# Performance work log

Measured on AMD Instinct MI355X. Metric: run time of the kernel, lower is better.

## Reference

```python
import jax, jax.numpy as jnp
import numpy as np

B, A, N_IN, N_POINTS = 64, 256, 512, 2048


def _sq_cdist(u, v):
    # |u_i - v_j|^2 via expansion, abs() as in the torch original
    d = -2.0 * (u @ v.T) + (u * u).sum(1)[:, None] + (v * v).sum(1)[None, :]
    return jnp.abs(d)


def setup_inputs() -> dict:
    key = jax.random.key(0)
    k1, k2, k3, k4 = jax.random.split(key, 4)
    x = jax.random.normal(k1, (B, A, N_IN), dtype=jnp.float32)
    atom_mask = jax.random.bernoulli(k2, 0.8, (B, A))  # ragged valid-atom mask
    inducing_points = jax.random.normal(k3, (N_POINTS, N_IN), dtype=jnp.float32)
    gamma = (1.0 + 0.25 * jax.random.normal(k4, (N_IN,), dtype=jnp.float32)) * np.sqrt(N_IN).astype(np.float32)
    return {"x": x, "atom_mask": atom_mask, "inducing_points": inducing_points, "gamma": gamma}


def reference(x, atom_mask, inducing_points, gamma):
    b, a, n_in = x.shape
    m = atom_mask.astype(x.dtype)                      # [B, A]
    mf = m[..., None]                                  # [B, A, 1]
    n = m.sum()
    # masked mean / unbiased std over valid atoms (torch .std is ddof=1)
    mean = (x * mf).sum((0, 1)) / n                    # [n_in]
    var = (((x - mean) ** 2) * mf).sum((0, 1)) / (n - 1.0)
    std = jnp.sqrt(var) + 1e-5                         # [n_in]
    xn = (x - mean) / std * mf                         # zero out padded atoms

    g2 = gamma ** 2 + 0.001                            # [n_in]
    z = (xn / g2).reshape(b * a, n_in)                 # [N, n_in]
    zi = inducing_points / g2                          # [M, n_in]

    Kx = jnp.exp(-_sq_cdist(z, zi))                    # [N, M]
    Kind = jnp.exp(-_sq_cdist(zi, zi))                 # [M, M]
    Kinv = jnp.linalg.inv(Kind + 0.05 * jnp.eye(Kind.shape[0], dtype=x.dtype))

    t = Kx @ Kinv                                      # [N, M]
    x_new = ((t @ inducing_points) * std + mean).reshape(b, a, n_in) * mf
    var_out = (1.0 - (t * Kx).sum(-1)).reshape(b, a) * m
    return x_new, var_out
```

## Files before the change

### kernel.cpp

```cpp
#include <hip/hip_runtime.h>
#include <math.h>
#include <stdint.h>

namespace {

constexpr int NROW = 16384;
constexpr int NF   = 512;
constexpr int MIND = 2048;
constexpr float CC = 0.98f;

typedef _Float16 half8 __attribute__((ext_vector_type(8)));
typedef _Float16 half4v __attribute__((ext_vector_type(4)));
typedef float floatx4 __attribute__((ext_vector_type(4)));

__device__ __forceinline__ void gload16(const void* g, void* l) {
  __builtin_amdgcn_global_load_lds(
      (__attribute__((address_space(1))) void*)g,
      (__attribute__((address_space(3))) void*)l, 16, 0, 0);
}

#define MEMFENCE asm volatile("" ::: "memory")
#define GATE(N) asm volatile("s_waitcnt vmcnt(" #N ")" ::: "memory")

__global__ __launch_bounds__(256) void stats_kernel(
    const float* __restrict__ x, const int* __restrict__ mask,
    float* __restrict__ sum, float* __restrict__ sumsq, float* __restrict__ cnt)
{
  const int t = threadIdx.x;
  const int row0 = blockIdx.x * 64;
  float s0 = 0.f, s1 = 0.f, q0 = 0.f, q1 = 0.f, c = 0.f;
  for (int r = 0; r < 64; ++r) {
    const int row = row0 + r;
    const float m = (mask[row] != 0) ? 1.f : 0.f;
    const float v0 = x[(size_t)row * NF + t];
    const float v1 = x[(size_t)row * NF + t + 256];
    s0 += m * v0; q0 += m * v0 * v0;
    s1 += m * v1; q1 += m * v1 * v1;
    c += m;
  }
  atomicAdd(&sum[t], s0);        atomicAdd(&sum[t + 256], s1);
  atomicAdd(&sumsq[t], q0);      atomicAdd(&sumsq[t + 256], q1);
  if (t == 0) atomicAdd(cnt, c);
}

__global__ __launch_bounds__(256) void finalize_stats(
    const float* __restrict__ sum, const float* __restrict__ sumsq,
    const float* __restrict__ cnt, const float* __restrict__ gamma,
    float* __restrict__ meanv, float* __restrict__ stdv,
    float* __restrict__ zsv, float* __restrict__ giv)
{
  const int f = blockIdx.x * 256 + threadIdx.x;
  const float n = cnt[0];
  const float mu = sum[f] / n;
  const float var = (sumsq[f] - sum[f] * mu) / (n - 1.0f);
  const float sd = sqrtf(var) + 1e-5f;
  const float g = gamma[f];
  const float g2 = g * g + 0.001f;
  meanv[f] = mu;
  stdv[f]  = sd;
  zsv[f]   = 1.0f / (sd * g2);
  giv[f]   = 1.0f / g2;
}

__global__ __launch_bounds__(256) void make_z(
    const float* __restrict__ x, const int* __restrict__ mask,
    const float* __restrict__ ip, const float* __restrict__ meanv,
    const float* __restrict__ zsv, const float* __restrict__ giv,
    _Float16* __restrict__ Zh, _Float16* __restrict__ Zih,
    float* __restrict__ rnorm, float* __restrict__ cnorm)
{
  const int row = blockIdx.x;
  const int t = threadIdx.x;
  float v0, v1;
  if (row < NROW) {
    const float m = (mask[row] != 0) ? 1.f : 0.f;
    v0 = (x[(size_t)row * NF + t      ] - meanv[t      ]) * zsv[t      ] * m;
    v1 = (x[(size_t)row * NF + t + 256] - meanv[t + 256]) * zsv[t + 256] * m;
    const _Float16 h0 = (_Float16)v0, h1 = (_Float16)v1;
    Zh[(size_t)row * NF + t] = h0;
    Zh[(size_t)row * NF + t + 256] = h1;
    v0 = (float)h0; v1 = (float)h1;
  } else {
    const int r = row - NROW;
    v0 = ip[(size_t)r * NF + t      ] * giv[t      ];
    v1 = ip[(size_t)r * NF + t + 256] * giv[t + 256];
    const _Float16 h0 = (_Float16)v0, h1 = (_Float16)v1;
    Zih[(size_t)r * NF + t] = h0;
    Zih[(size_t)r * NF + t + 256] = h1;
    v0 = (float)h0; v1 = (float)h1;
  }
  float nrm = v0 * v0 + v1 * v1;
  #pragma unroll
  for (int off = 32; off; off >>= 1) nrm += __shfl_xor(nrm, off);
  __shared__ float red[4];
  if ((t & 63) == 0) red[t >> 6] = nrm;
  __syncthreads();
  if (t == 0) {
    const float s = red[0] + red[1] + red[2] + red[3];
    if (row < NROW) rnorm[row] = s; else cnorm[row - NROW] = s;
  }
}

template <int PASS>
__global__ __launch_bounds__(512, 2) void mfma_gemm256f(
    const _Float16* __restrict__ A, const _Float16* __restrict__ B, int K,
    const float* __restrict__ rn, const float* __restrict__ cn,
    _Float16* __restrict__ DKout, float* __restrict__ Cf,
    const _Float16* __restrict__ DK, const float* __restrict__ u,
    float* __restrict__ varacc,
    const float* __restrict__ colsumR, const float* __restrict__ stdv,
    const float* __restrict__ meanv, const int* __restrict__ mask)
{
  __shared__ __align__(16) _Float16 Asmem[4][256 * 32];
  __shared__ __align__(16) _Float16 Bsmem[4][256 * 32];

  const int tid = threadIdx.x;
  const int w = tid >> 6, L = tid & 63;
  const int wm = w >> 2, wn = w & 3;
  const int lq = L >> 4, lr = L & 15;
  int bn, bm;
  if constexpr (PASS == 0) {
    const int wgid = blockIdx.y * 8 + blockIdx.x;
    const int xcd = wgid & 7, q = wgid >> 3;
    bm = xcd + 8 * (q >> 3);
    bn = q & 7;
  } else {
    const int wgid = blockIdx.y * 10 + blockIdx.x;
    const int xcd = wgid & 7, q = wgid >> 3;
    bm = xcd + 8 * (q / 10);
    bn = q % 10;
  }
  const int NT = K >> 5;

  const int srow  = tid >> 2;
  const int sslot = tid & 3;
  const int gslot = sslot ^ ((tid >> 3) & 3);
  const _Float16* Ag = A + (size_t)(bm * 256 + srow) * K + gslot * 8;
  const _Float16* Bg = B + (size_t)(bn * 256 + srow) * K + gslot * 8;
  const size_t rstride = (size_t)128 * K;
  const int ldst = srow * 32 + sslot * 8;

  const int fswz = (lq ^ ((lr >> 1) & 3)) * 8;
  const int aoff = (wm * 128 + lr) * 32 + fswz;
  const int boff = (wn * 64  + lr) * 32 + fswz;

  floatx4 acc[8][4] = {};

  auto stageA = [&](int t) {
    _Float16* dst = Asmem[t & 3] + ldst;
    const _Float16* src = Ag + (size_t)t * 32;
    gload16(src, dst);
    gload16(src + rstride, dst + 128 * 32);
  };
  auto stageB = [&](int t) {
    _Float16* dst = Bsmem[t & 3] + ldst;
    const _Float16* src = Bg + (size_t)t * 32;
    gload16(src, dst);
    gload16(src + rstride, dst + 128 * 32);
  };

  stageA(0); stageB(0);
  if (NT > 1) { stageA(1); stageB(1); }
  if (NT > 2) { stageA(2); stageB(2); }
  if (NT > 2)      { GATE(8); }
  else if (NT > 1) { GATE(4); }
  else             { GATE(0); }
  __builtin_amdgcn_s_barrier();
  MEMFENCE;

  for (int t = 0; t < NT; ++t) {
    const _Float16* As = Asmem[t & 3];
    const _Float16* Bs = Bsmem[t & 3];
    half8 af[4], bf[4], af2[4];

    #pragma unroll
    for (int mi = 0; mi < 4; ++mi) af[mi] = *(const half8*)&As[aoff + mi * 512];
    #pragma unroll
    for (int ni = 0; ni < 4; ++ni) bf[ni] = *(const half8*)&Bs[boff + ni * 512];
    if (t + 3 < NT) stageA(t + 3);
    MEMFENCE;
    __builtin_amdgcn_s_barrier();
    MEMFENCE;
    __builtin_amdgcn_s_setprio(1);
    #pragma unroll
    for (int mi = 0; mi < 4; ++mi)
      #pragma unroll
      for (int ni = 0; ni < 4; ++ni)
        acc[mi][ni] = __builtin_amdgcn_mfma_f32_16x16x32_f16(
            af[mi], bf[ni], acc[mi][ni], 0, 0, 0);
    __builtin_amdgcn_s_setprio(0);

    #pragma unroll
    for (int mi = 0; mi < 4; ++mi)
      af2[mi] = *(const half8*)&As[aoff + (mi + 4) * 512];
    if (t + 3 < NT) stageB(t + 3);
    if (t + 4 <= NT)      { GATE(8); }
    else if (t + 3 == NT) { GATE(4); }
    else if (t + 2 == NT) { GATE(0); }
    __builtin_amdgcn_s_barrier();
    MEMFENCE;
    __builtin_amdgcn_s_setprio(1);
    #pragma unroll
    for (int mi = 0; mi < 4; ++mi)
      #pragma unroll
      for (int ni = 0; ni < 4; ++ni)
        acc[mi + 4][ni] = __builtin_amdgcn_mfma_f32_16x16x32_f16(
            af2[mi], bf[ni], acc[mi + 4][ni], 0, 0, 0);
    __builtin_amdgcn_s_setprio(0);
  }

  const int grb = bm * 256 + wm * 128;
  const int gcb = bn * 256 + wn * 64;

  if constexpr (PASS == 0) {
    if (bm < NROW / 256) {
      #pragma unroll
      for (int mi = 0; mi < 8; ++mi)
        #pragma unroll
        for (int e = 0; e < 4; ++e) {
          const int gr = grb + mi * 16 + lq * 4 + e;
          const float rni = rn[gr];
          #pragma unroll
          for (int ni = 0; ni < 4; ++ni) {
            const int gc = gcb + ni * 16 + lr;
            const float d = rni + cn[gc] - 2.f * acc[mi][ni][e];
            DKout[(size_t)gr * MIND + gc] = (_Float16)(expf(-fabsf(d)) - CC);
          }
        }
    } else {
      #pragma unroll
      for (int mi = 0; mi < 8; ++mi)
        #pragma unroll
        for (int e = 0; e < 4; ++e) {
          const int gr = grb + mi * 16 + lq * 4 + e;
          const int gr2 = gr - NROW;
          const float rni = rn[gr];
          #pragma unroll
          for (int ni = 0; ni < 4; ++ni) {
            const int gc = gcb + ni * 16 + lr;
            const float d = rni + cn[gc] - 2.f * acc[mi][ni][e];
            float kx = expf(-fabsf(d));
            if (gr2 == gc) kx += 0.05f;
            Cf[(size_t)gr2 * MIND + gc] = kx;
          }
        }
    }
  } else {
    if (bn < MIND / 256) {
      #pragma unroll
      for (int mi = 0; mi < 8; ++mi)
        #pragma unroll
        for (int e = 0; e < 4; ++e) {
          const int gr = grb + mi * 16 + lq * 4 + e;
          float partial = 0.f;
          #pragma unroll
          for (int ni = 0; ni < 4; ++ni) {
            const int gc = gcb + ni * 16 + lr;
            const float tv = acc[mi][ni][e] + CC * u[gc];
            partial += tv * (CC + (float)DK[(size_t)gr * MIND + gc]);
          }
          partial += __shfl_xor(partial, 1);
          partial += __shfl_xor(partial, 2);
          partial += __shfl_xor(partial, 4);
          partial += __shfl_xor(partial, 8);
          if (lr == 0) atomicAdd(&varacc[gr], partial);
        }
    } else {
      const int gcb3 = (bn - MIND / 256) * 256 + wn * 64;
      #pragma unroll
      for (int mi = 0; mi < 8; ++mi)
        #pragma unroll
        for (int e = 0; e < 4; ++e) {
          const int gr = grb + mi * 16 + lq * 4 + e;
          const float mrow = (mask[gr] != 0) ? 1.f : 0.f;
          #pragma unroll
          for (int ni = 0; ni < 4; ++ni) {
            const int gc3 = gcb3 + ni * 16 + lr;
            const float v = acc[mi][ni][e] + CC * colsumR[gc3];
            Cf[(size_t)gr * NF + gc3] = (v * stdv[gc3] + meanv[gc3]) * mrow;
          }
        }
    }
  }
}

__global__ __launch_bounds__(256) void gemm_f32(
    const float* __restrict__ A, const float* __restrict__ B,
    float* __restrict__ C, int M, int N, int K)
{
  constexpr int BM = 64, BN = 64, BK = 16;
  const int tid = threadIdx.x;
  const int tx = tid % 16, ty = tid / 16;
  const int bn = blockIdx.x, bm = blockIdx.y;
  __shared__ float As[BK][BM + 4];
  __shared__ float Bs[BK][BN + 4];
  float acc[4][4] = {};
  const float* Ag = A + (size_t)bm * BM * K;
  const float* Bg = B + bn * BN;
  for (int k0 = 0; k0 < K; k0 += BK) {
    {
      const int r = tid >> 2, c4 = (tid & 3) << 2;
      const float4 av = *(const float4*)(Ag + (size_t)r * K + k0 + c4);
      As[c4 + 0][r] = av.x; As[c4 + 1][r] = av.y;
      As[c4 + 2][r] = av.z; As[c4 + 3][r] = av.w;
      const int kr = tid / 16, nc = (tid % 16) << 2;
      *(float4*)&Bs[kr][nc] = *(const float4*)(Bg + (size_t)(k0 + kr) * N + nc);
    }
    __syncthreads();
    #pragma unroll
    for (int kk = 0; kk < BK; ++kk) {
      const float4 a4 = *(const float4*)&As[kk][ty * 4];
      const float4 b4 = *(const float4*)&Bs[kk][tx * 4];
      const float a[4] = {a4.x, a4.y, a4.z, a4.w};
      const float b[4] = {b4.x, b4.y, b4.z, b4.w};
      #pragma unroll
      for (int i = 0; i < 4; ++i)
        #pragma unroll
        for (int j = 0; j < 4; ++j) acc[i][j] += a[i] * b[j];
    }
    __syncthreads();
  }
  #pragma unroll
  for (int i = 0; i < 4; ++i) {
    float4 o4; o4.x = acc[i][0]; o4.y = acc[i][1]; o4.z = acc[i][2]; o4.w = acc[i][3];
    *(float4*)(C + (size_t)(bm * BM + ty * 4 + i) * N + bn * BN + tx * 4) = o4;
  }
}


__global__ __launch_bounds__(256) void gj_diag(
    float* __restrict__ A, float* __restrict__ Pall, int k)
{
  const int o = k * 64;
  __shared__ float D[64][68];
  const int t = threadIdx.x;
  #pragma unroll
  for (int l = 0; l < 4; ++l) {
    const int v = t + l * 256;
    const int r = v >> 4, c4 = (v & 15) << 2;
    *(float4*)&D[r][c4] = *(const float4*)(A + (size_t)(o + r) * MIND + o + c4);
  }
  __syncthreads();
  const int i = t >> 2, c0 = (t & 3) * 16;
  for (int s = 0; s < 64; ++s) {
    const float p = 1.0f / D[s][s];
    if (t < 64 && t != s) D[s][t] *= p;
    __syncthreads();
    if (i != s) {
      const float f = D[i][s];
      #pragma unroll
      for (int c = c0; c < c0 + 16; c += 4) {
        float4 ds = *(const float4*)&D[s][c];
        float4 di = *(const float4*)&D[i][c];
        di.x -= f * ds.x; di.y -= f * ds.y; di.z -= f * ds.z; di.w -= f * ds.w;
        *(float4*)&D[i][c] = di;
      }
      if (s >= c0 && s < c0 + 16) D[i][s] = -f * p;
    }
    if (t == 0) D[s][s] = p;
    __syncthreads();
  }
  float* P = Pall + k * 4096;
  #pragma unroll
  for (int l = 0; l < 4; ++l) {
    const int v = t + l * 256;
    const int r = v >> 4, c4 = (v & 15) << 2;
    const float4 dv = *(const float4*)&D[r][c4];
    *(float4*)(P + r * 64 + c4) = dv;
    *(float4*)(A + (size_t)(o + r) * MIND + o + c4) = dv;
  }
}

__global__ __launch_bounds__(256) void gj_prep(
    const float* __restrict__ A, const float* __restrict__ Pall,
    float* __restrict__ CP, float* __restrict__ Bsave, int k)
{
  const int o = k * 64;
  const int t = threadIdx.x;
  if (blockIdx.x >= 32) {
    const int j0 = (blockIdx.x - 32) * 64;
    #pragma unroll
    for (int l = 0; l < 4; ++l) {
      const int v = t + l * 256;
      const int r = v >> 4, c4 = (v & 15) << 2;
      *(float4*)(Bsave + r * MIND + j0 + c4) =
          *(const float4*)(A + (size_t)(o + r) * MIND + j0 + c4);
    }
    return;
  }
  const int i0 = blockIdx.x * 64;
  if (i0 == o) return;
  const float* P = Pall + k * 4096;
  __shared__ float At[64][68];
  __shared__ float Pl[64][68];
  #pragma unroll
  for (int l = 0; l < 4; ++l) {
    const int v = t + l * 256;
    const int r = v >> 4, c4 = (v & 15) << 2;
    const float4 av = *(const float4*)(A + (size_t)(i0 + r) * MIND + o + c4);
    At[c4 + 0][r] = av.x; At[c4 + 1][r] = av.y;
    At[c4 + 2][r] = av.z; At[c4 + 3][r] = av.w;
    *(float4*)&Pl[r][c4] = *(const float4*)(P + r * 64 + c4);
  }
  __syncthreads();
  const int ty = t >> 4, tx = t & 15;
  float acc[4][4] = {};
  for (int s = 0; s < 64; ++s) {
    const float4 a4 = *(const float4*)&At[s][ty * 4];
    const float4 b4 = *(const float4*)&Pl[s][tx * 4];
    const float a[4] = {a4.x, a4.y, a4.z, a4.w};
    const float b[4] = {b4.x, b4.y, b4.z, b4.w};
    #pragma unroll
    for (int i = 0; i < 4; ++i)
      #pragma unroll
      for (int j = 0; j < 4; ++j) acc[i][j] += a[i] * b[j];
  }
  #pragma unroll
  for (int i = 0; i < 4; ++i) {
    float4 o4; o4.x = acc[i][0]; o4.y = acc[i][1]; o4.z = acc[i][2]; o4.w = acc[i][3];
    *(float4*)(CP + (i0 + ty * 4 + i) * 64 + tx * 4) = o4;
  }
}

__global__ __launch_bounds__(256) void gj_apply(
    float* __restrict__ A, float* __restrict__ Pall,
    const float* __restrict__ CP, const float* __restrict__ Bsave, int k)
{
  const int o = k * 64;
  const int i0 = blockIdx.y * 64, j0 = blockIdx.x * 64;
  const int t = threadIdx.x;

  if (i0 == o && j0 == o) return;

  if (j0 == o) {
    #pragma unroll
    for (int l = 0; l < 4; ++l) {
      const int v = t + l * 256;
      const int r = v >> 4, c4 = (v & 15) << 2;
      float4 x = *(const float4*)(CP + (i0 + r) * 64 + c4);
      x.x = -x.x; x.y = -x.y; x.z = -x.z; x.w = -x.w;
      *(float4*)(A + (size_t)(i0 + r) * MIND + o + c4) = x;
    }
    return;
  }

  __shared__ float S1[64 * 68];
  __shared__ float S2[64 * 68];
  #define DD(r, c) S1[(r) * 68 + (c)]

  const bool isrow = (i0 == o);
  const float* Lsrc = isrow ? (Pall + k * 4096) : (CP + i0 * 64);
  #pragma unroll
  for (int l = 0; l < 4; ++l) {
    const int v = t + l * 256;
    const int r = v >> 4, c4 = (v & 15) << 2;
    const float4 lv = *(const float4*)(Lsrc + r * 64 + c4);
    S1[(c4 + 0) * 68 + r] = lv.x; S1[(c4 + 1) * 68 + r] = lv.y;
    S1[(c4 + 2) * 68 + r] = lv.z; S1[(c4 + 3) * 68 + r] = lv.w;
    *(float4*)&S2[r * 68 + c4] = *(const float4*)(Bsave + r * MIND + j0 + c4);
  }
  __syncthreads();
  const int ty = t >> 4, tx = t & 15;
  float acc[4][4] = {};
  for (int s = 0; s < 64; ++s) {
    const float4 a4 = *(const float4*)&S1[s * 68 + ty * 4];
    const float4 b4 = *(const float4*)&S2[s * 68 + tx * 4];
    const float a[4] = {a4.x, a4.y, a4.z, a4.w};
    const float b[4] = {b4.x, b4.y, b4.z, b4.w};
    #pragma unroll
    for (int i = 0; i < 4; ++i)
      #pragma unroll
      for (int j = 0; j < 4; ++j) acc[i][j] += a[i] * b[j];
  }

  if (isrow) {
    #pragma unroll
    for (int i = 0; i < 4; ++i) {
      float4 o4; o4.x = acc[i][0]; o4.y = acc[i][1]; o4.z = acc[i][2]; o4.w = acc[i][3];
      *(float4*)(A + (size_t)(o + ty * 4 + i) * MIND + j0 + tx * 4) = o4;
    }
    return;
  }

  const bool isdiagnext = (i0 == o + 64) && (j0 == o + 64);
  if (!isdiagnext) {
    #pragma unroll
    for (int i = 0; i < 4; ++i) {
      float* cp = A + (size_t)(i0 + ty * 4 + i) * MIND + j0 + tx * 4;
      float4 cv = *(const float4*)cp;
      cv.x -= acc[i][0]; cv.y -= acc[i][1]; cv.z -= acc[i][2]; cv.w -= acc[i][3];
      *(float4*)cp = cv;
    }
    return;
  }

  __syncthreads();
  #pragma unroll
  for (int i = 0; i < 4; ++i) {
    const float4 cv = *(const float4*)(A + (size_t)(i0 + ty * 4 + i) * MIND + j0 + tx * 4);
    DD(ty * 4 + i, tx * 4 + 0) = cv.x - acc[i][0];
    DD(ty * 4 + i, tx * 4 + 1) = cv.y - acc[i][1];
    DD(ty * 4 + i, tx * 4 + 2) = cv.z - acc[i][2];
    DD(ty * 4 + i, tx * 4 + 3) = cv.w - acc[i][3];
  }
  __syncthreads();
  const int di = t >> 2, c0 = (t & 3) * 16;
  for (int s = 0; s < 64; ++s) {
    const float p = 1.0f / DD(s, s);
    if (t < 64 && t != s) DD(s, t) *= p;
    __syncthreads();
    if (di != s) {
      const float f = DD(di, s);
      #pragma unroll
      for (int c = c0; c < c0 + 16; c += 4) {
        float4 ds = *(const float4*)&DD(s, c);
        float4 dv = *(const float4*)&DD(di, c);
        dv.x -= f * ds.x; dv.y -= f * ds.y; dv.z -= f * ds.z; dv.w -= f * ds.w;
        *(float4*)&DD(di, c) = dv;
      }
      if (s >= c0 && s < c0 + 16) DD(di, s) = -f * p;
    }
    if (t == 0) DD(s, s) = p;
    __syncthreads();
  }
  float* Pn = Pall + (k + 1) * 4096;
  #pragma unroll
  for (int l = 0; l < 4; ++l) {
    const int v = t + l * 256;
    const int r = v >> 4, c4 = (v & 15) << 2;
    const float4 dv = *(const float4*)&DD(r, c4);
    *(float4*)(Pn + r * 64 + c4) = dv;
    *(float4*)(A + (size_t)(i0 + r) * MIND + j0 + c4) = dv;
  }
  #undef DD
}

__global__ __launch_bounds__(256) void rowsum_cast(
    const float* __restrict__ Ai, float* __restrict__ u,
    _Float16* __restrict__ Kih)
{
  const int row = blockIdx.x * 4 + (threadIdx.x >> 6);
  const int lane = threadIdx.x & 63;
  const float* src = Ai + (size_t)row * MIND;
  _Float16* dst = Kih + (size_t)row * MIND;
  float s = 0.f;
  #pragma unroll
  for (int it = 0; it < 8; ++it) {
    const int c = it * 256 + lane * 4;
    const float4 v = *(const float4*)(src + c);
    s += v.x + v.y + v.z + v.w;
    half4v h; h.x = (_Float16)v.x; h.y = (_Float16)v.y;
    h.z = (_Float16)v.z; h.w = (_Float16)v.w;
    *(half4v*)(dst + c) = h;
  }
  #pragma unroll
  for (int off = 32; off; off >>= 1) s += __shfl_xor(s, off);
  if (lane == 0) u[row] = s;
}

__global__ __launch_bounds__(256) void transpose_colsum(
    const float* __restrict__ R, _Float16* __restrict__ Rt,
    float* __restrict__ cs)
{
  __shared__ float T[64][65];
  __shared__ float psum[4][64];
  const int j0 = blockIdx.x * 64;
  const int f0 = blockIdx.y * 64;
  const int t = threadIdx.x;
  #pragma unroll
  for (int l = 0; l < 16; ++l) {
    const int idx = t + l * 256;
    T[idx >> 6][idx & 63] = R[(size_t)(j0 + (idx >> 6)) * NF + f0 + (idx & 63)];
  }
  __syncthreads();
  #pragma unroll
  for (int l = 0; l < 16; ++l) {
    const int idx = t + l * 256;
    const int fr = idx >> 6, jc = idx & 63;
    Rt[(size_t)(f0 + fr) * MIND + j0 + jc] = (_Float16)T[jc][fr];
  }
  const int f = t & 63, q = t >> 6;
  float s = 0.f;
  #pragma unroll
  for (int j = q * 16; j < q * 16 + 16; ++j) s += T[j][f];
  psum[q][f] = s;
  __syncthreads();
  if (t < 64) atomicAdd(&cs[f0 + t], psum[0][t] + psum[1][t] + psum[2][t] + psum[3][t]);
}

__global__ __launch_bounds__(256) void var_finalize(
    const float* __restrict__ varacc, const int* __restrict__ mask,
    float* __restrict__ outv)
{
  const int i = blockIdx.x * 256 + threadIdx.x;
  const float m = (mask[i] != 0) ? 1.f : 0.f;
  outv[i] = (1.0f - varacc[i]) * m;
}

}

extern "C" void kernel_launch(void* const* d_in, const int* in_sizes, int n_in,
                              void* d_out, int out_size, void* d_ws, size_t ws_size,
                              hipStream_t stream)
{
  (void)in_sizes; (void)n_in; (void)out_size; (void)ws_size;
  const float* x     = (const float*)d_in[0];
  const int*   mask  = (const int*)d_in[1];
  const float* ip    = (const float*)d_in[2];
  const float* gamma = (const float*)d_in[3];
  float* out = (float*)d_out;

  float* w       = (float*)d_ws;
  float* sum     = w;
  float* sumsq   = w + 512;
  float* cnt     = w + 1024;
  float* varacc  = w + 1536;
  float* colsumR = w + 17920;
  float* meanv   = w + 18432;
  float* stdv    = w + 18944;
  float* zsv     = w + 19456;
  float* giv     = w + 19968;
  float* rnorm   = w + 20480;
  float* cnorm   = w + 36864;
  float* u       = w + 38912;
  float* Ai      = w + 40960;
  float* R       = w + 4235264;
  float* Pall    = w + 5283840;
  float* CP      = w + 5414912;
  float* Bsave   = w + 5545984;
  _Float16* hb   = (_Float16*)(w + 5677056);
  _Float16* Zh   = hb;
  _Float16* Zih  = hb + 8388608;
  _Float16* DK   = hb + 9437184;
  _Float16* Kih  = hb + 42991616;
  _Float16* Rt   = hb + 47185920;

  hipMemsetAsync(w, 0, 18432 * sizeof(float), stream);

  stats_kernel<<<256, 256, 0, stream>>>(x, mask, sum, sumsq, cnt);
  finalize_stats<<<2, 256, 0, stream>>>(sum, sumsq, cnt, gamma, meanv, stdv, zsv, giv);
  make_z<<<NROW + MIND, 256, 0, stream>>>(x, mask, ip, meanv, zsv, giv, Zh, Zih, rnorm, cnorm);

  mfma_gemm256f<0><<<dim3(MIND / 256, (NROW + MIND) / 256), 512, 0, stream>>>(
      Zh, Zih, NF, rnorm, cnorm,
      DK, Ai, nullptr, nullptr, nullptr, nullptr, nullptr, nullptr, nullptr);

  gj_diag<<<1, 256, 0, stream>>>(Ai, Pall, 0);
  gj_prep<<<64, 256, 0, stream>>>(Ai, Pall, CP, Bsave, 0);
  for (int k = 0; k < 32; ++k) {
    gj_apply<<<dim3(32, 32), 256, 0, stream>>>(Ai, Pall, CP, Bsave, k);
    if (k < 31) gj_prep<<<64, 256, 0, stream>>>(Ai, Pall, CP, Bsave, k + 1);
  }

  gemm_f32<<<dim3(NF / 64, MIND / 64), 256, 0, stream>>>(Ai, ip, R, MIND, NF, MIND);
  transpose_colsum<<<dim3(MIND / 64, NF / 64), 256, 0, stream>>>(R, Rt, colsumR);
  rowsum_cast<<<MIND / 4, 256, 0, stream>>>(Ai, u, Kih);

  mfma_gemm256f<1><<<dim3((MIND + NF) / 256, NROW / 256), 512, 0, stream>>>(
      DK, Kih, MIND, nullptr, nullptr,
      nullptr, out, DK, u, varacc, colsumR, stdv, meanv, mask);

  var_finalize<<<NROW / 256, 256, 0, stream>>>(varacc, mask, out + (size_t)NROW * NF);
}
```

Measured before the change: 2.084 ms.

## Fuse Gauss-Jordan inversion steps into one persistent kernel with grid barriers

Replaces the ~66 separate launches of the block Gauss-Jordan inversion, plus the following f32 GEMM, transpose/colsum and rowsum-cast kernels, with one persistent 512-block kernel. Each step is separated by a software grid barrier built on atomics. The goal is to remove per-launch overhead and launch gaps on the serialized inversion chain. In exchange, each block handles two apply tiles per step, and correctness depends on all 512 blocks being co-resident, otherwise the barrier can deadlock. The barrier counters sit in the zeroed workspace area.

Result: slower. 6.857 ms (+229.0%).

```diff
diff --git a/kernel.cpp b/kernel.cpp
--- a/kernel.cpp
+++ b/kernel.cpp
@@ -8,6 +8,7 @@
 constexpr int NF   = 512;
 constexpr int MIND = 2048;
 constexpr float CC = 0.98f;
+constexpr int GJ_BLOCKS = 512;
 
 typedef _Float16 half8 __attribute__((ext_vector_type(8)));
 typedef _Float16 half4v __attribute__((ext_vector_type(4)));
@@ -21,6 +22,27 @@
 
 #define MEMFENCE asm volatile("" ::: "memory")
 #define GATE(N) asm volatile("s_waitcnt vmcnt(" #N ")" ::: "memory")
+
+__device__ __forceinline__ void gbar(int* cnt, int* gen, int nb) {
+  __syncthreads();
+  if (threadIdx.x == 0) {
+    __threadfence();
+    const int g = __hip_atomic_load(gen, __ATOMIC_RELAXED,
+                                    __HIP_MEMORY_SCOPE_AGENT);
+    if (__hip_atomic_fetch_add(cnt, 1, __ATOMIC_ACQ_REL,
+                               __HIP_MEMORY_SCOPE_AGENT) == nb - 1) {
+      __hip_atomic_store(cnt, 0, __ATOMIC_RELAXED, __HIP_MEMORY_SCOPE_AGENT);
+      __hip_atomic_fetch_add(gen, 1, __ATOMIC_RELEASE,
+                             __HIP_MEMORY_SCOPE_AGENT);
+    } else {
+      while (__hip_atomic_load(gen, __ATOMIC_ACQUIRE,
+                               __HIP_MEMORY_SCOPE_AGENT) == g)
+        __builtin_amdgcn_s_sleep(16);
+    }
+    __threadfence();
+  }
+  __syncthreads();
+}
 
 __global__ __launch_bounds__(256) void stats_kernel(
     const float* __restrict__ x, const int* __restrict__ mask,
@@ -284,80 +306,37 @@
   }
 }
 
-__global__ __launch_bounds__(256) void gemm_f32(
-    const float* __restrict__ A, const float* __restrict__ B,
-    float* __restrict__ C, int M, int N, int K)
-{
-  constexpr int BM = 64, BN = 64, BK = 16;
-  const int tid = threadIdx.x;
-  const int tx = tid % 16, ty = tid / 16;
-  const int bn = blockIdx.x, bm = blockIdx.y;
-  __shared__ float As[BK][BM + 4];
-  __shared__ float Bs[BK][BN + 4];
-  float acc[4][4] = {};
-  const float* Ag = A + (size_t)bm * BM * K;
-  const float* Bg = B + bn * BN;
-  for (int k0 = 0; k0 < K; k0 += BK) {
-    {
-      const int r = tid >> 2, c4 = (tid & 3) << 2;
-      const float4 av = *(const float4*)(Ag + (size_t)r * K + k0 + c4);
-      As[c4 + 0][r] = av.x; As[c4 + 1][r] = av.y;
-      As[c4 + 2][r] = av.z; As[c4 + 3][r] = av.w;
-      const int kr = tid / 16, nc = (tid % 16) << 2;
-      *(float4*)&Bs[kr][nc] = *(const float4*)(Bg + (size_t)(k0 + kr) * N + nc);
-    }
-    __syncthreads();
-    #pragma unroll
-    for (int kk = 0; kk < BK; ++kk) {
-      const float4 a4 = *(const float4*)&As[kk][ty * 4];
-      const float4 b4 = *(const float4*)&Bs[kk][tx * 4];
-      const float a[4] = {a4.x, a4.y, a4.z, a4.w};
-      const float b[4] = {b4.x, b4.y, b4.z, b4.w};
-      #pragma unroll
-      for (int i = 0; i < 4; ++i)
-        #pragma unroll
-        for (int j = 0; j < 4; ++j) acc[i][j] += a[i] * b[j];
-    }
-    __syncthreads();
-  }
-  #pragma unroll
-  for (int i = 0; i < 4; ++i) {
-    float4 o4; o4.x = acc[i][0]; o4.y = acc[i][1]; o4.z = acc[i][2]; o4.w = acc[i][3];
-    *(float4*)(C + (size_t)(bm * BM + ty * 4 + i) * N + bn * BN + tx * 4) = o4;
-  }
-}
-
-
-__global__ __launch_bounds__(256) void gj_diag(
-    float* __restrict__ A, float* __restrict__ Pall, int k)
+
+__device__ __forceinline__ void d_gj_diag(
+    float* __restrict__ A, float* __restrict__ Pall, int k, float* S1)
 {
   const int o = k * 64;
-  __shared__ float D[64][68];
   const int t = threadIdx.x;
+  #define D(r, c) S1[(r) * 68 + (c)]
   #pragma unroll
   for (int l = 0; l < 4; ++l) {
     const int v = t + l * 256;
     const int r = v >> 4, c4 = (v & 15) << 2;
-    *(float4*)&D[r][c4] = *(const float4*)(A + (size_t)(o + r) * MIND + o + c4);
+    *(float4*)&D(r, c4) = *(const float4*)(A + (size_t)(o + r) * MIND + o + c4);
   }
   __syncthreads();
   const int i = t >> 2, c0 = (t & 3) * 16;
   for (int s = 0; s < 64; ++s) {
-    const float p = 1.0f / D[s][s];
-    if (t < 64 && t != s) D[s][t] *= p;
+    const float p = 1.0f / D(s, s);
+    if (t < 64 && t != s) D(s, t) *= p;
     __syncthreads();
     if (i != s) {
-      const float f = D[i][s];
+      const float f = D(i, s);
       #pragma unroll
       for (int c = c0; c < c0 + 16; c += 4) {
-        float4 ds = *(const float4*)&D[s][c];
-        float4 di = *(const float4*)&D[i][c];
+        float4 ds = *(const float4*)&D(s, c);
+        float4 di = *(const float4*)&D(i, c);
         di.x -= f * ds.x; di.y -= f * ds.y; di.z -= f * ds.z; di.w -= f * ds.w;
-        *(float4*)&D[i][c] = di;
+        *(float4*)&D(i, c) = di;
       }
-      if (s >= c0 && s < c0 + 16) D[i][s] = -f * p;
-    }
-    if (t == 0) D[s][s] = p;
+      if (s >= c0 && s < c0 + 16) D(i, s) = -f * p;
+    }
+    if (t == 0) D(s, s) = p;
     __syncthreads();
   }
   float* P = Pall + k * 4096;
@@ -365,20 +344,22 @@
   for (int l = 0; l < 4; ++l) {
     const int v = t + l * 256;
     const int r = v >> 4, c4 = (v & 15) << 2;
-    const float4 dv = *(const float4*)&D[r][c4];
+    const float4 dv = *(const float4*)&D(r, c4);
     *(float4*)(P + r * 64 + c4) = dv;
     *(float4*)(A + (size_t)(o + r) * MIND + o + c4) = dv;
   }
-}
-
-__global__ __launch_bounds__(256) void gj_prep(
-    const float* __restrict__ A, const float* __restrict__ Pall,
-    float* __restrict__ CP, float* __restrict__ Bsave, int k)
+  #undef D
+}
+
+__device__ __forceinline__ void d_gj_prep(
+    float* __restrict__ A, float* __restrict__ Pall,
+    float* __restrict__ CP, float* __restrict__ Bsave, int k, int b,
+    float* S1, float* S2)
 {
   const int o = k * 64;
   const int t = threadIdx.x;
-  if (blockIdx.x >= 32) {
-    const int j0 = (blockIdx.x - 32) * 64;
+  if (b >= 32) {
+    const int j0 = (b - 32) * 64;
     #pragma unroll
     for (int l = 0; l < 4; ++l) {
       const int v = t + l * 256;
@@ -388,32 +369,30 @@
     }
     return;
   }
-  const int i0 = blockIdx.x * 64;
+  const int i0 = b * 64;
   if (i0 == o) return;
   const float* P = Pall + k * 4096;
-  __shared__ float At[64][68];
-  __shared__ float Pl[64][68];
   #pragma unroll
   for (int l = 0; l < 4; ++l) {
     const int v = t + l * 256;
     const int r = v >> 4, c4 = (v & 15) << 2;
     const float4 av = *(const float4*)(A + (size_t)(i0 + r) * MIND + o + c4);
-    At[c4 + 0][r] = av.x; At[c4 + 1][r] = av.y;
-    At[c4 + 2][r] = av.z; At[c4 + 3][r] = av.w;
-    *(float4*)&Pl[r][c4] = *(const float4*)(P + r * 64 + c4);
+    S1[(c4 + 0) * 68 + r] = av.x; S1[(c4 + 1) * 68 + r] = av.y;
+    S1[(c4 + 2) * 68 + r] = av.z; S1[(c4 + 3) * 68 + r] = av.w;
+    *(float4*)&S2[r * 68 + c4] = *(const float4*)(P + r * 64 + c4);
   }
   __syncthreads();
   const int ty = t >> 4, tx = t & 15;
   float acc[4][4] = {};
   for (int s = 0; s < 64; ++s) {
-    const float4 a4 = *(const float4*)&At[s][ty * 4];
-    const float4 b4 = *(const float4*)&Pl[s][tx * 4];
+    const float4 a4 = *(const float4*)&S1[s * 68 + ty * 4];
+    const float4 b4 = *(const float4*)&S2[s * 68 + tx * 4];
     const float a[4] = {a4.x, a4.y, a4.z, a4.w};
-    const float b[4] = {b4.x, b4.y, b4.z, b4.w};
+    const float bb[4] = {b4.x, b4.y, b4.z, b4.w};
     #pragma unroll
     for (int i = 0; i < 4; ++i)
       #pragma unroll
-      for (int j = 0; j < 4; ++j) acc[i][j] += a[i] * b[j];
+      for (int j = 0; j < 4; ++j) acc[i][j] += a[i] * bb[j];
   }
   #pragma unroll
   for (int i = 0; i < 4; ++i) {
@@ -422,12 +401,12 @@
   }
 }
 
-__global__ __launch_bounds__(256) void gj_apply(
+__device__ __forceinline__ void d_gj_apply(
     float* __restrict__ A, float* __restrict__ Pall,
-    const float* __restrict__ CP, const float* __restrict__ Bsave, int k)
+    const float* __restrict__ CP, const float* __restrict__ Bsave, int k,
+    int i0, int j0, float* S1, float* S2)
 {
   const int o = k * 64;
-  const int i0 = blockIdx.y * 64, j0 = blockIdx.x * 64;
   const int t = threadIdx.x;
 
   if (i0 == o && j0 == o) return;
@@ -444,10 +423,8 @@
     return;
   }
 
-  __shared__ float S1[64 * 68];
-  __shared__ float S2[64 * 68];
+  __syncthreads();
   #define DD(r, c) S1[(r) * 68 + (c)]
-
   const bool isrow = (i0 == o);
   const float* Lsrc = isrow ? (Pall + k * 4096) : (CP + i0 * 64);
   #pragma unroll
@@ -466,11 +443,11 @@
     const float4 a4 = *(const float4*)&S1[s * 68 + ty * 4];
     const float4 b4 = *(const float4*)&S2[s * 68 + tx * 4];
     const float a[4] = {a4.x, a4.y, a4.z, a4.w};
-    const float b[4] = {b4.x, b4.y, b4.z, b4.w};
+    const float bb[4] = {b4.x, b4.y, b4.z, b4.w};
     #pragma unroll
     for (int i = 0; i < 4; ++i)
       #pragma unroll
-      for (int j = 0; j < 4; ++j) acc[i][j] += a[i] * b[j];
+      for (int j = 0; j < 4; ++j) acc[i][j] += a[i] * bb[j];
   }
 
   if (isrow) {
@@ -523,7 +500,7 @@
     if (t == 0) DD(s, s) = p;
     __syncthreads();
   }
-  float* Pn = Pall + (k + 1) * 4096;
+  float* Pn = Pall + (size_t)(k + 1) * 4096;
   #pragma unroll
   for (int l = 0; l < 4; ++l) {
     const int v = t + l * 256;
@@ -535,11 +512,51 @@
   #undef DD
 }
 
-__global__ __launch_bounds__(256) void rowsum_cast(
+__device__ __forceinline__ void d_gemm_f32(
+    const float* __restrict__ A, const float* __restrict__ B,
+    float* __restrict__ C, int bm, int bn, float* S1, float* S2)
+{
+  constexpr int BK = 16;
+  const int tid = threadIdx.x;
+  const int tx = tid % 16, ty = tid / 16;
+  float acc[4][4] = {};
+  const float* Ag = A + (size_t)bm * 64 * MIND;
+  const float* Bg = B + bn * 64;
+  for (int k0 = 0; k0 < MIND; k0 += BK) {
+    {
+      const int r = tid >> 2, c4 = (tid & 3) << 2;
+      const float4 av = *(const float4*)(Ag + (size_t)r * MIND + k0 + c4);
+      S1[(c4 + 0) * 68 + r] = av.x; S1[(c4 + 1) * 68 + r] = av.y;
+      S1[(c4 + 2) * 68 + r] = av.z; S1[(c4 + 3) * 68 + r] = av.w;
+      const int kr = tid / 16, nc = (tid % 16) << 2;
+      *(float4*)&S2[kr * 68 + nc] = *(const float4*)(Bg + (size_t)(k0 + kr) * NF + nc);
+    }
+    __syncthreads();
+    #pragma unroll
+    for (int kk = 0; kk < BK; ++kk) {
+      const float4 a4 = *(const float4*)&S1[kk * 68 + ty * 4];
+      const float4 b4 = *(const float4*)&S2[kk * 68 + tx * 4];
+      const float a[4] = {a4.x, a4.y, a4.z, a4.w};
+      const float bb[4] = {b4.x, b4.y, b4.z, b4.w};
+      #pragma unroll
+      for (int i = 0; i < 4; ++i)
+        #pragma unroll
+        for (int j = 0; j < 4; ++j) acc[i][j] += a[i] * bb[j];
+    }
+    __syncthreads();
+  }
+  #pragma unroll
+  for (int i = 0; i < 4; ++i) {
+    float4 o4; o4.x = acc[i][0]; o4.y = acc[i][1]; o4.z = acc[i][2]; o4.w = acc[i][3];
+    *(float4*)(C + (size_t)(bm * 64 + ty * 4 + i) * NF + bn * 64 + tx * 4) = o4;
+  }
+}
+
+__device__ __forceinline__ void d_rowsum_cast(
     const float* __restrict__ Ai, float* __restrict__ u,
-    _Float16* __restrict__ Kih)
-{
-  const int row = blockIdx.x * 4 + (threadIdx.x >> 6);
+    _Float16* __restrict__ Kih, int rg)
+{
+  const int row = rg * 4 + (threadIdx.x >> 6);
   const int lane = threadIdx.x & 63;
   const float* src = Ai + (size_t)row * MIND;
   _Float16* dst = Kih + (size_t)row * MIND;
@@ -558,34 +575,74 @@
   if (lane == 0) u[row] = s;
 }
 
-__global__ __launch_bounds__(256) void transpose_colsum(
+__device__ __forceinline__ void d_transpose_colsum(
     const float* __restrict__ R, _Float16* __restrict__ Rt,
-    float* __restrict__ cs)
-{
-  __shared__ float T[64][65];
-  __shared__ float psum[4][64];
-  const int j0 = blockIdx.x * 64;
-  const int f0 = blockIdx.y * 64;
+    float* __restrict__ cs, int j0, int f0, float* S1, float* S2)
+{
   const int t = threadIdx.x;
   #pragma unroll
   for (int l = 0; l < 16; ++l) {
     const int idx = t + l * 256;
-    T[idx >> 6][idx & 63] = R[(size_t)(j0 + (idx >> 6)) * NF + f0 + (idx & 63)];
+    S1[(idx >> 6) * 65 + (idx & 63)] =
+        R[(size_t)(j0 + (idx >> 6)) * NF + f0 + (idx & 63)];
   }
   __syncthreads();
   #pragma unroll
   for (int l = 0; l < 16; ++l) {
     const int idx = t + l * 256;
     const int fr = idx >> 6, jc = idx & 63;
-    Rt[(size_t)(f0 + fr) * MIND + j0 + jc] = (_Float16)T[jc][fr];
+    Rt[(size_t)(f0 + fr) * MIND + j0 + jc] = (_Float16)S1[jc * 65 + fr];
   }
   const int f = t & 63, q = t >> 6;
   float s = 0.f;
   #pragma unroll
-  for (int j = q * 16; j < q * 16 + 16; ++j) s += T[j][f];
-  psum[q][f] = s;
-  __syncthreads();
-  if (t < 64) atomicAdd(&cs[f0 + t], psum[0][t] + psum[1][t] + psum[2][t] + psum[3][t]);
+  for (int j = q * 16; j < q * 16 + 16; ++j) s += S1[j * 65 + f];
+  S2[q * 64 + f] = s;
+  __syncthreads();
+  if (t < 64)
+    atomicAdd(&cs[f0 + t], S2[0 * 64 + t] + S2[1 * 64 + t] +
+                           S2[2 * 64 + t] + S2[3 * 64 + t]);
+}
+
+__global__ __launch_bounds__(256, 2) void fused_gj(
+    float* __restrict__ A, float* __restrict__ Pall,
+    float* __restrict__ CP, float* __restrict__ Bsave,
+    const float* __restrict__ ip, float* __restrict__ R,
+    _Float16* __restrict__ Rt, float* __restrict__ colsumR,
+    float* __restrict__ u, _Float16* __restrict__ Kih,
+    int* __restrict__ bcnt, int* __restrict__ bgen)
+{
+  __shared__ float S1[64 * 68];
+  __shared__ float S2[64 * 68];
+  const int b = blockIdx.x;
+
+  if (b == 0) d_gj_diag(A, Pall, 0, S1);
+  gbar(bcnt, bgen, GJ_BLOCKS);
+  if (b < 64) d_gj_prep(A, Pall, CP, Bsave, 0, b, S1, S2);
+  gbar(bcnt, bgen, GJ_BLOCKS);
+
+  for (int k = 0; k < 32; ++k) {
+    {
+      const int t0 = b, t1 = b + 512;
+      d_gj_apply(A, Pall, CP, Bsave, k, (t0 >> 5) * 64, (t0 & 31) * 64, S1, S2);
+      d_gj_apply(A, Pall, CP, Bsave, k, (t1 >> 5) * 64, (t1 & 31) * 64, S1, S2);
+    }
+    gbar(bcnt, bgen, GJ_BLOCKS);
+    if (k < 31) {
+      if (b < 64) d_gj_prep(A, Pall, CP, Bsave, k + 1, b, S1, S2);
+      gbar(bcnt, bgen, GJ_BLOCKS);
+    }
+  }
+
+  if (b < 256) {
+    d_gemm_f32(A, ip, R, b >> 3, b & 7, S1, S2);
+  } else {
+    d_rowsum_cast(A, u, Kih, (b - 256) * 2);
+    d_rowsum_cast(A, u, Kih, (b - 256) * 2 + 1);
+  }
+  gbar(bcnt, bgen, GJ_BLOCKS);
+  if (b < 256)
+    d_transpose_colsum(R, Rt, colsumR, (b & 31) * 64, (b >> 5) * 64, S1, S2);
 }
 
 __global__ __launch_bounds__(256) void var_finalize(
@@ -614,6 +671,8 @@
   float* sum     = w;
   float* sumsq   = w + 512;
   float* cnt     = w + 1024;
+  int*   bcnt    = (int*)(w + 1040);
+  int*   bgen    = (int*)(w + 1041);
   float* varacc  = w + 1536;
   float* colsumR = w + 17920;
   float* meanv   = w + 18432;
@@ -645,16 +704,8 @@
       Zh, Zih, NF, rnorm, cnorm,
       DK, Ai, nullptr, nullptr, nullptr, nullptr, nullptr, nullptr, nullptr);
 
-  gj_diag<<<1, 256, 0, stream>>>(Ai, Pall, 0);
-  gj_prep<<<64, 256, 0, stream>>>(Ai, Pall, CP, Bsave, 0);
-  for (int k = 0; k < 32; ++k) {
-    gj_apply<<<dim3(32, 32), 256, 0, stream>>>(Ai, Pall, CP, Bsave, k);
-    if (k < 31) gj_prep<<<64, 256, 0, stream>>>(Ai, Pall, CP, Bsave, k + 1);
-  }
-
-  gemm_f32<<<dim3(NF / 64, MIND / 64), 256, 0, stream>>>(Ai, ip, R, MIND, NF, MIND);
-  transpose_colsum<<<dim3(MIND / 64, NF / 64), 256, 0, stream>>>(R, Rt, colsumR);
-  rowsum_cast<<<MIND / 4, 256, 0, stream>>>(Ai, u, Kih);
+  fused_gj<<<GJ_BLOCKS, 256, 0, stream>>>(
+      Ai, Pall, CP, Bsave, ip, R, Rt, colsumR, u, Kih, bcnt, bgen);
 
   mfma_gemm256f<1><<<dim3((MIND + NF) / 256, NROW / 256), 512, 0, stream>>>(
       DK, Kih, MIND, nullptr, nullptr,
```

## Compute Kinv·ip with fp16 MFMA GEMM producing transposed output directly

Applied to the files above, without the earlier changes.

Replaces the fp32 SIMT GEMM (Kinv @ inducing_points) and the separate transpose/colsum kernel with an fp16 MFMA GEMM computing ip^T·Kinv^T, writing Rt directly. This relies on Kinv being symmetric. The column-sum term is now computed separately as u^T·ip in a small reduction kernel. The cost is an extra transpose-to-fp16 of ip and a lower-precision product, and the new GEMM launches only 16 workgroups, so it uses few CUs.

Result: faster. 2.032 ms (-2.5%).

```diff
diff --git a/kernel.cpp b/kernel.cpp
--- a/kernel.cpp
+++ b/kernel.cpp
@@ -101,6 +101,27 @@
   }
 }
 
+__global__ __launch_bounds__(256) void ip_t16(
+    const float* __restrict__ ip, _Float16* __restrict__ ipTh)
+{
+  __shared__ float T[64][65];
+  const int j0 = blockIdx.x * 64;
+  const int f0 = blockIdx.y * 64;
+  const int t = threadIdx.x;
+  #pragma unroll
+  for (int l = 0; l < 16; ++l) {
+    const int idx = t + l * 256;
+    T[idx >> 6][idx & 63] = ip[(size_t)(j0 + (idx >> 6)) * NF + f0 + (idx & 63)];
+  }
+  __syncthreads();
+  #pragma unroll
+  for (int l = 0; l < 16; ++l) {
+    const int idx = t + l * 256;
+    const int fr = idx >> 6, jc = idx & 63;
+    ipTh[(size_t)(f0 + fr) * MIND + j0 + jc] = (_Float16)T[jc][fr];
+  }
+}
+
 template <int PASS>
 __global__ __launch_bounds__(512, 2) void mfma_gemm256f(
     const _Float16* __restrict__ A, const _Float16* __restrict__ B, int K,
@@ -124,11 +145,15 @@
     const int xcd = wgid & 7, q = wgid >> 3;
     bm = xcd + 8 * (q >> 3);
     bn = q & 7;
-  } else {
+  } else if constexpr (PASS == 1) {
     const int wgid = blockIdx.y * 10 + blockIdx.x;
     const int xcd = wgid & 7, q = wgid >> 3;
     bm = xcd + 8 * (q / 10);
     bn = q % 10;
+  } else {
+    const int wgid = blockIdx.y * 8 + blockIdx.x;
+    bm = wgid >> 3;
+    bn = wgid & 7;
   }
   const int NT = K >> 5;
 
@@ -245,7 +270,7 @@
           }
         }
     }
-  } else {
+  } else if constexpr (PASS == 1) {
     if (bn < MIND / 256) {
       #pragma unroll
       for (int mi = 0; mi < 8; ++mi)
@@ -281,49 +306,18 @@
           }
         }
     }
-  }
-}
-
-__global__ __launch_bounds__(256) void gemm_f32(
-    const float* __restrict__ A, const float* __restrict__ B,
-    float* __restrict__ C, int M, int N, int K)
-{
-  constexpr int BM = 64, BN = 64, BK = 16;
-  const int tid = threadIdx.x;
-  const int tx = tid % 16, ty = tid / 16;
-  const int bn = blockIdx.x, bm = blockIdx.y;
-  __shared__ float As[BK][BM + 4];
-  __shared__ float Bs[BK][BN + 4];
-  float acc[4][4] = {};
-  const float* Ag = A + (size_t)bm * BM * K;
-  const float* Bg = B + bn * BN;
-  for (int k0 = 0; k0 < K; k0 += BK) {
-    {
-      const int r = tid >> 2, c4 = (tid & 3) << 2;
-      const float4 av = *(const float4*)(Ag + (size_t)r * K + k0 + c4);
-      As[c4 + 0][r] = av.x; As[c4 + 1][r] = av.y;
-      As[c4 + 2][r] = av.z; As[c4 + 3][r] = av.w;
-      const int kr = tid / 16, nc = (tid % 16) << 2;
-      *(float4*)&Bs[kr][nc] = *(const float4*)(Bg + (size_t)(k0 + kr) * N + nc);
-    }
-    __syncthreads();
-    #pragma unroll
-    for (int kk = 0; kk < BK; ++kk) {
-      const float4 a4 = *(const float4*)&As[kk][ty * 4];
-      const float4 b4 = *(const float4*)&Bs[kk][tx * 4];
-      const float a[4] = {a4.x, a4.y, a4.z, a4.w};
-      const float b[4] = {b4.x, b4.y, b4.z, b4.w};
-      #pragma unroll
-      for (int i = 0; i < 4; ++i)
+  } else {
+    #pragma unroll
+    for (int mi = 0; mi < 8; ++mi)
+      #pragma unroll
+      for (int e = 0; e < 4; ++e) {
+        const int gr = grb + mi * 16 + lq * 4 + e;
         #pragma unroll
-        for (int j = 0; j < 4; ++j) acc[i][j] += a[i] * b[j];
-    }
-    __syncthreads();
-  }
-  #pragma unroll
-  for (int i = 0; i < 4; ++i) {
-    float4 o4; o4.x = acc[i][0]; o4.y = acc[i][1]; o4.z = acc[i][2]; o4.w = acc[i][3];
-    *(float4*)(C + (size_t)(bm * BM + ty * 4 + i) * N + bn * BN + tx * 4) = o4;
+        for (int ni = 0; ni < 4; ++ni) {
+          const int gc = gcb + ni * 16 + lr;
+          DKout[(size_t)gr * MIND + gc] = (_Float16)acc[mi][ni][e];
+        }
+      }
   }
 }
 
@@ -558,34 +552,20 @@
   if (lane == 0) u[row] = s;
 }
 
-__global__ __launch_bounds__(256) void transpose_colsum(
-    const float* __restrict__ R, _Float16* __restrict__ Rt,
+__global__ __launch_bounds__(256) void colsum_u(
+    const float* __restrict__ ip, const float* __restrict__ u,
     float* __restrict__ cs)
 {
-  __shared__ float T[64][65];
-  __shared__ float psum[4][64];
-  const int j0 = blockIdx.x * 64;
-  const int f0 = blockIdx.y * 64;
+  const int b = blockIdx.x;
   const int t = threadIdx.x;
-  #pragma unroll
-  for (int l = 0; l < 16; ++l) {
-    const int idx = t + l * 256;
-    T[idx >> 6][idx & 63] = R[(size_t)(j0 + (idx >> 6)) * NF + f0 + (idx & 63)];
-  }
-  __syncthreads();
-  #pragma unroll
-  for (int l = 0; l < 16; ++l) {
-    const int idx = t + l * 256;
-    const int fr = idx >> 6, jc = idx & 63;
-    Rt[(size_t)(f0 + fr) * MIND + j0 + jc] = (_Float16)T[jc][fr];
-  }
-  const int f = t & 63, q = t >> 6;
-  float s = 0.f;
-  #pragma unroll
-  for (int j = q * 16; j < q * 16 + 16; ++j) s += T[j][f];
-  psum[q][f] = s;
-  __syncthreads();
-  if (t < 64) atomicAdd(&cs[f0 + t], psum[0][t] + psum[1][t] + psum[2][t] + psum[3][t]);
+  float s0 = 0.f, s1 = 0.f;
+  for (int r = 0; r < 64; ++r) {
+    const int row = b * 64 + r;
+    const float uk = u[row];
+    s0 += uk * ip[(size_t)row * NF + t];
+    s1 += uk * ip[(size_t)row * NF + t + 256];
+  }
+  atomicAdd(&cs[t], s0); atomicAdd(&cs[t + 256], s1);
 }
 
 __global__ __launch_bounds__(256) void var_finalize(
@@ -624,7 +604,7 @@
   float* cnorm   = w + 36864;
   float* u       = w + 38912;
   float* Ai      = w + 40960;
-  float* R       = w + 4235264;
+  _Float16* ipTh = (_Float16*)(w + 4235264);
   float* Pall    = w + 5283840;
   float* CP      = w + 5414912;
   float* Bsave   = w + 5545984;
@@ -640,6 +620,7 @@
   stats_kernel<<<256, 256, 0, stream>>>(x, mask, sum, sumsq, cnt);
   finalize_stats<<<2, 256, 0, stream>>>(sum, sumsq, cnt, gamma, meanv, stdv, zsv, giv);
   make_z<<<NROW + MIND, 256, 0, stream>>>(x, mask, ip, meanv, zsv, giv, Zh, Zih, rnorm, cnorm);
+  ip_t16<<<dim3(MIND / 64, NF / 64), 256, 0, stream>>>(ip, ipTh);
 
   mfma_gemm256f<0><<<dim3(MIND / 256, (NROW + MIND) / 256), 512, 0, stream>>>(
       Zh, Zih, NF, rnorm, cnorm,
@@ -652,9 +633,11 @@
     if (k < 31) gj_prep<<<64, 256, 0, stream>>>(Ai, Pall, CP, Bsave, k + 1);
   }
 
-  gemm_f32<<<dim3(NF / 64, MIND / 64), 256, 0, stream>>>(Ai, ip, R, MIND, NF, MIND);
-  transpose_colsum<<<dim3(MIND / 64, NF / 64), 256, 0, stream>>>(R, Rt, colsumR);
   rowsum_cast<<<MIND / 4, 256, 0, stream>>>(Ai, u, Kih);
+  mfma_gemm256f<2><<<dim3(8, 2), 512, 0, stream>>>(
+      ipTh, Kih, MIND, nullptr, nullptr,
+      Rt, nullptr, nullptr, nullptr, nullptr, nullptr, nullptr, nullptr, nullptr);
+  colsum_u<<<MIND / 64, 256, 0, stream>>>(ip, u, colsumR);
 
   mfma_gemm256f<1><<<dim3((MIND + NF) / 256, NROW / 256), 512, 0, stream>>>(
       DK, Kih, MIND, nullptr, nullptr,
```
